# Optimization experiments

Hardware: AMD Instinct MI355X
Metric: run time of the kernel (lower is better)

The kernel has to match this reference:

```python
import jax, jax.numpy as jnp
import numpy as np

N_TAU = 100  # steps per delay: dt = tau / N_TAU (backward code uses dt = 0.01*tau)


def F_model(x, y, t, W1, W2, b):
    # F(x(t), x(t - tau), t); t enters the signature but this Model is autonomous,
    # matching the repo's example models.
    return jnp.tanh(W1 @ x + W2 @ y + b)


def setup_inputs() -> dict:
    key = jax.random.key(0)
    d = 512
    k1, k2, k3, k4 = jax.random.split(key, 4)
    scale = 1.0 / np.sqrt(d).astype(np.float32)
    x_0 = jax.random.normal(k1, (d,), dtype=jnp.float32)
    W1 = jax.random.normal(k2, (d, d), dtype=jnp.float32) * scale
    W2 = jax.random.normal(k3, (d, d), dtype=jnp.float32) * scale
    b = jax.random.normal(k4, (d,), dtype=jnp.float32)
    tau = jnp.ones((), dtype=jnp.float32)  # time delay; dt = 0.01 * tau
    N = 2000  # = floor(T / dt) with T = 20, tau = 1
    return {"x_0": x_0, "tau": tau, "W1": W1, "W2": W2, "b": b, "N": N}


def reference(x_0, tau, W1, W2, b, N):
    """Forward-Euler DDE solve of x'(t) = F(x(t), x(t - tau), t), x(t) = x_0 for t <= 0.
    Returns the trajectory as a [d, N+1] array (kth column = state at step k),
    matching DDE_Solver's x_Trajectory layout."""
    d = x_0.shape[0]
    M = N_TAU + 1  # ring buffer holds the last N_tau+1 states
    dt = 0.01 * tau

    buf0 = jnp.zeros((d, M), dtype=x_0.dtype).at[:, 0].set(x_0)

    def step(buf, j):
        x_j = buf[:, j % M]
        # delayed state x(t_j - tau) = x_{j - N_tau}; (j - N_tau) % M == (j + 1) % M
        y_hist = buf[:, (j + 1) % M]
        y_j = jnp.where(j >= N_TAU, y_hist, x_0)  # pre-history: x(t) = x_0
        t_j = j * dt
        x_jp1 = x_j + dt * F_model(x_j, y_j, t_j, W1, W2, b)
        buf = buf.at[:, (j + 1) % M].set(x_jp1)
        return buf, x_jp1

    _, ys = jax.lax.scan(step, buf0, jnp.arange(N))  # ys: [N, d]
    return jnp.concatenate([x_0[:, None], ys.T], axis=1)  # [d, N+1]
```

## Files before the change

kernel.cpp:

```cpp
#include <hip/hip_runtime.h>


#define D    512
#define NTAU 100
#define M    112
#define NWGS 128

typedef unsigned long long u64;

__device__ __forceinline__ float lo_f(u64 v){ union{unsigned u; float f;} c; c.u=(unsigned)v; return c.f; }
__device__ __forceinline__ u64 pack_rec(unsigned tag, float x){ union{unsigned u; float f;} c; c.f=x; return ((u64)tag<<32)|(u64)c.u; }
__device__ __forceinline__ u64 ag_ld(const u64* p){
    return __hip_atomic_load(p, __ATOMIC_RELAXED, __HIP_MEMORY_SCOPE_AGENT);
}
__device__ __forceinline__ void ag_st(u64* p, u64 v){
    __hip_atomic_store(p, v, __ATOMIC_RELAXED, __HIP_MEMORY_SCOPE_AGENT);
}

__global__ __launch_bounds__(64, 1) void ndde_r4(
    const float* __restrict__ x0p, const float* __restrict__ taup,
    const float* __restrict__ W1,  const float* __restrict__ W2,
    const float* __restrict__ bb,  const int* __restrict__ Np,
    float* __restrict__ out, u64* __restrict__ ring)
{
    const int lane    = threadIdx.x & 63;
    const int rowbase = blockIdx.x * 4;
    const int N       = Np[0];
    const float dt    = 0.01f * taup[0];

    float w1v[4][8], w2v[4][8];
    #pragma unroll
    for (int r = 0; r < 4; ++r){
        const float* p1 = W1 + (size_t)(rowbase + r) * D + lane;
        const float* p2 = W2 + (size_t)(rowbase + r) * D + lane;
        #pragma unroll
        for (int i = 0; i < 8; ++i){
            w1v[r][i] = p1[64 * i];
            w2v[r][i] = p2[64 * i];
        }
    }
    #pragma unroll
    for (int r = 0; r < 4; ++r){
        #pragma unroll
        for (int i = 0; i < 8; ++i)
            asm volatile("" : "+v"(w1v[r][i]), "+v"(w2v[r][i]));
    }

    float xv0[8];
    #pragma unroll
    for (int i = 0; i < 8; ++i) xv0[i] = x0p[64 * i + lane];
    float yp[4], a0, a1, a2, a3;
    {
        float t[4];
        #pragma unroll
        for (int r = 0; r < 4; ++r){
            float sy = 0.f, st = 0.f;
            #pragma unroll
            for (int i = 0; i < 8; ++i){
                sy = fmaf(w2v[r][i], xv0[i], sy);
                st = fmaf(w1v[r][i], xv0[i], st);
            }
            yp[r] = sy; t[r] = st;
        }
        a0 = t[0] + yp[0]; a1 = t[1] + yp[1];
        a2 = t[2] + yp[2]; a3 = t[3] + yp[3];
    }
    #pragma unroll
    for (int off = 32; off >= 1; off >>= 1){
        a0 += __shfl_xor(a0, off, 64);
        a1 += __shfl_xor(a1, off, 64);
        a2 += __shfl_xor(a2, off, 64);
        a3 += __shfl_xor(a3, off, 64);
    }

    float xloc = 0.f, bval = 0.f;
    if (lane < 4){
        const int row = rowbase + lane;
        xloc = x0p[row];
        bval = bb[row];
        out[(size_t)row * (N + 1)] = xloc;
        if (N >= 1){
            const float acc = (lane == 0) ? a0 : (lane == 1) ? a1
                            : (lane == 2) ? a2 : a3;
            const float x1 = xloc + dt * tanhf(acc + bval);
            xloc = x1;
            ag_st(ring + D + row, pack_rec(2u, x1));
            out[(size_t)row * (N + 1) + 1] = x1;
        }
    }

    u64 xr[8], yr[8];
    int sx = 1, sp = 2, sy = 1;
    bool dead = false;

    for (int j = 1; j < N && !dead; ++j){
        const bool needy  = (j > NTAU);
        const unsigned tx = (unsigned)(j + 1);
        const u64* px = ring + (size_t)sx * D + lane;

        if (needy){
            const u64* py = ring + (size_t)sy * D + lane;
            #pragma unroll
            for (int i = 0; i < 8; ++i) yr[i] = ag_ld(py + 64 * i);
        }

        int it = 0;
        for (;;){
            #pragma unroll
            for (int i = 0; i < 8; ++i) xr[i] = ag_ld(px + 64 * i);
            bool ok = true;
            #pragma unroll
            for (int i = 0; i < 8; ++i) ok &= ((unsigned)(xr[i] >> 32) == tx);
            if (__all(ok)) break;
            if (++it > (1 << 22)){ dead = true; break; }
        }

        if (needy){
            const unsigned ty = (unsigned)(j - NTAU + 1);
            bool ok = true;
            #pragma unroll
            for (int i = 0; i < 8; ++i) ok &= ((unsigned)(yr[i] >> 32) == ty);
            if (!__all(ok)){
                const u64* py = ring + (size_t)sy * D + lane;
                int it2 = 0;
                for (;;){
                    #pragma unroll
                    for (int i = 0; i < 8; ++i) yr[i] = ag_ld(py + 64 * i);
                    bool ok2 = true;
                    #pragma unroll
                    for (int i = 0; i < 8; ++i) ok2 &= ((unsigned)(yr[i] >> 32) == ty);
                    if (__all(ok2)) break;
                    if (++it2 > (1 << 22)){ dead = true; break; }
                }
            }
        }

        if (needy){
            a0 = a1 = a2 = a3 = 0.f;
            #pragma unroll
            for (int i = 0; i < 8; ++i){
                const float xf = lo_f(xr[i]), yf = lo_f(yr[i]);
                a0 = fmaf(w1v[0][i], xf, a0); a0 = fmaf(w2v[0][i], yf, a0);
                a1 = fmaf(w1v[1][i], xf, a1); a1 = fmaf(w2v[1][i], yf, a1);
                a2 = fmaf(w1v[2][i], xf, a2); a2 = fmaf(w2v[2][i], yf, a2);
                a3 = fmaf(w1v[3][i], xf, a3); a3 = fmaf(w2v[3][i], yf, a3);
            }
        } else {
            a0 = yp[0]; a1 = yp[1]; a2 = yp[2]; a3 = yp[3];
            #pragma unroll
            for (int i = 0; i < 8; ++i){
                const float xf = lo_f(xr[i]);
                a0 = fmaf(w1v[0][i], xf, a0);
                a1 = fmaf(w1v[1][i], xf, a1);
                a2 = fmaf(w1v[2][i], xf, a2);
                a3 = fmaf(w1v[3][i], xf, a3);
            }
        }

        #pragma unroll
        for (int off = 32; off >= 1; off >>= 1){
            a0 += __shfl_xor(a0, off, 64);
            a1 += __shfl_xor(a1, off, 64);
            a2 += __shfl_xor(a2, off, 64);
            a3 += __shfl_xor(a3, off, 64);
        }

        if (lane < 4){
            const float acc = (lane == 0) ? a0 : (lane == 1) ? a1
                            : (lane == 2) ? a2 : a3;
            const float xn = xloc + dt * tanhf(acc + bval);
            xloc = xn;
            const int row = rowbase + lane;
            ag_st(ring + (size_t)sp * D + row, pack_rec(tx + 1, xn));
            out[(size_t)row * (N + 1) + (j + 1)] = xn;
        }

        sx = (sx == M - 1) ? 0 : sx + 1;
        sp = (sp == M - 1) ? 0 : sp + 1;
        if (j >= NTAU + 1) sy = (sy == M - 1) ? 0 : sy + 1;
    }
}

extern "C" void kernel_launch(void* const* d_in, const int* in_sizes, int n_in,
                              void* d_out, int out_size, void* d_ws, size_t ws_size,
                              hipStream_t stream)
{
    const float* x0  = (const float*)d_in[0];
    const float* tau = (const float*)d_in[1];
    const float* W1  = (const float*)d_in[2];
    const float* W2  = (const float*)d_in[3];
    const float* b   = (const float*)d_in[4];
    const int*   Np  = (const int*)  d_in[5];

    u64* ring = (u64*)d_ws;

    hipLaunchKernelGGL(ndde_r4, dim3(NWGS), dim3(64), 0, stream,
                       x0, tau, W1, W2, b, Np, (float*)d_out, ring);
}
```

Before: 3.627 ms.

## Halve workgroups to 64 with 8 rows each and precompute delayed term locally

Each workgroup now owns 8 rows instead of 4, so 64 workgroups take part in the per-step spin-wait synchronization instead of 128. Each workgroup also keeps a private copy of recent states in workspace and computes the W2·y delayed contribution off the critical path after publishing its new state. This removes the second polled ring read from the step's critical path. The cost is twice the register footprint for the weights and twice the per-lane dot-product work per step, plus extra global writes and reads for the private history. The spin-timeout limits are also lowered.

```diff
diff --git a/kernel.cpp b/kernel.cpp
--- a/kernel.cpp
+++ b/kernel.cpp
@@ -1,10 +1,11 @@
 #include <hip/hip_runtime.h>
 
 
-#define D    512
-#define NTAU 100
-#define M    112
-#define NWGS 128
+#define D     512
+#define NTAU  100
+#define M     112
+#define HSLOT 101
+#define NW    64
 
 typedef unsigned long long u64;
 
@@ -16,21 +17,31 @@
 __device__ __forceinline__ void ag_st(u64* p, u64 v){
     __hip_atomic_store(p, v, __ATOMIC_RELAXED, __HIP_MEMORY_SCOPE_AGENT);
 }
-
-__global__ __launch_bounds__(64, 1) void ndde_r4(
+__device__ __forceinline__ float sel8(const float* a, int k){
+    float s = a[0];
+    s = (k == 1) ? a[1] : s;  s = (k == 2) ? a[2] : s;
+    s = (k == 3) ? a[3] : s;  s = (k == 4) ? a[4] : s;
+    s = (k == 5) ? a[5] : s;  s = (k == 6) ? a[6] : s;
+    s = (k == 7) ? a[7] : s;
+    return s;
+}
+
+__global__ __launch_bounds__(64, 1) void ndde_r5(
     const float* __restrict__ x0p, const float* __restrict__ taup,
     const float* __restrict__ W1,  const float* __restrict__ W2,
     const float* __restrict__ bb,  const int* __restrict__ Np,
-    float* __restrict__ out, u64* __restrict__ ring)
+    float* __restrict__ out, u64* __restrict__ ring,
+    float* __restrict__ hist, int use_hist)
 {
     const int lane    = threadIdx.x & 63;
-    const int rowbase = blockIdx.x * 4;
+    const int wb      = blockIdx.x;
+    const int rowbase = wb * 8;
     const int N       = Np[0];
     const float dt    = 0.01f * taup[0];
 
-    float w1v[4][8], w2v[4][8];
-    #pragma unroll
-    for (int r = 0; r < 4; ++r){
+    float w1v[8][8], w2v[8][8];
+    #pragma unroll
+    for (int r = 0; r < 8; ++r){
         const float* p1 = W1 + (size_t)(rowbase + r) * D + lane;
         const float* p2 = W2 + (size_t)(rowbase + r) * D + lane;
         #pragma unroll
@@ -40,7 +51,7 @@
         }
     }
     #pragma unroll
-    for (int r = 0; r < 4; ++r){
+    for (int r = 0; r < 8; ++r){
         #pragma unroll
         for (int i = 0; i < 8; ++i)
             asm volatile("" : "+v"(w1v[r][i]), "+v"(w2v[r][i]));
@@ -49,48 +60,43 @@
     float xv0[8];
     #pragma unroll
     for (int i = 0; i < 8; ++i) xv0[i] = x0p[64 * i + lane];
-    float yp[4], a0, a1, a2, a3;
-    {
-        float t[4];
-        #pragma unroll
-        for (int r = 0; r < 4; ++r){
-            float sy = 0.f, st = 0.f;
-            #pragma unroll
-            for (int i = 0; i < 8; ++i){
-                sy = fmaf(w2v[r][i], xv0[i], sy);
-                st = fmaf(w1v[r][i], xv0[i], st);
-            }
-            yp[r] = sy; t[r] = st;
-        }
-        a0 = t[0] + yp[0]; a1 = t[1] + yp[1];
-        a2 = t[2] + yp[2]; a3 = t[3] + yp[3];
+    float yp[8], a[8];
+    #pragma unroll
+    for (int r = 0; r < 8; ++r){
+        float sy = 0.f, st = 0.f;
+        #pragma unroll
+        for (int i = 0; i < 8; ++i){
+            sy = fmaf(w2v[r][i], xv0[i], sy);
+            st = fmaf(w1v[r][i], xv0[i], st);
+        }
+        yp[r] = sy; a[r] = st + sy;
     }
     #pragma unroll
     for (int off = 32; off >= 1; off >>= 1){
-        a0 += __shfl_xor(a0, off, 64);
-        a1 += __shfl_xor(a1, off, 64);
-        a2 += __shfl_xor(a2, off, 64);
-        a3 += __shfl_xor(a3, off, 64);
+        #pragma unroll
+        for (int r = 0; r < 8; ++r) a[r] += __shfl_xor(a[r], off, 64);
     }
 
     float xloc = 0.f, bval = 0.f;
-    if (lane < 4){
+    if (lane < 8){
         const int row = rowbase + lane;
         xloc = x0p[row];
         bval = bb[row];
         out[(size_t)row * (N + 1)] = xloc;
         if (N >= 1){
-            const float acc = (lane == 0) ? a0 : (lane == 1) ? a1
-                            : (lane == 2) ? a2 : a3;
-            const float x1 = xloc + dt * tanhf(acc + bval);
+            const float x1 = xloc + dt * tanhf(sel8(a, lane) + bval);
             xloc = x1;
             ag_st(ring + D + row, pack_rec(2u, x1));
             out[(size_t)row * (N + 1) + 1] = x1;
         }
     }
 
-    u64 xr[8], yr[8];
-    int sx = 1, sp = 2, sy = 1;
+    float* myh = hist + (size_t)wb * HSLOT * D;
+
+    u64 xr[8];
+    float xf[8];
+    int sx = 1, sp = 2, syr = 1;
+    int hw = 0, hr = 0;
     bool dead = false;
 
     for (int j = 1; j < N && !dead; ++j){
@@ -98,8 +104,9 @@
         const unsigned tx = (unsigned)(j + 1);
         const u64* px = ring + (size_t)sx * D + lane;
 
-        if (needy){
-            const u64* py = ring + (size_t)sy * D + lane;
+        u64 yr[8];
+        if (!use_hist && needy){
+            const u64* py = ring + (size_t)syr * D + lane;
             #pragma unroll
             for (int i = 0; i < 8; ++i) yr[i] = ag_ld(py + 64 * i);
         }
@@ -112,16 +119,18 @@
             #pragma unroll
             for (int i = 0; i < 8; ++i) ok &= ((unsigned)(xr[i] >> 32) == tx);
             if (__all(ok)) break;
-            if (++it > (1 << 22)){ dead = true; break; }
-        }
-
-        if (needy){
+            if (++it > (1 << 20)){ dead = true; break; }
+        }
+        #pragma unroll
+        for (int i = 0; i < 8; ++i) xf[i] = lo_f(xr[i]);
+
+        if (!use_hist && needy){
             const unsigned ty = (unsigned)(j - NTAU + 1);
             bool ok = true;
             #pragma unroll
             for (int i = 0; i < 8; ++i) ok &= ((unsigned)(yr[i] >> 32) == ty);
             if (!__all(ok)){
-                const u64* py = ring + (size_t)sy * D + lane;
+                const u64* py = ring + (size_t)syr * D + lane;
                 int it2 = 0;
                 for (;;){
                     #pragma unroll
@@ -130,54 +139,62 @@
                     #pragma unroll
                     for (int i = 0; i < 8; ++i) ok2 &= ((unsigned)(yr[i] >> 32) == ty);
                     if (__all(ok2)) break;
-                    if (++it2 > (1 << 22)){ dead = true; break; }
+                    if (++it2 > (1 << 20)){ dead = true; break; }
                 }
             }
-        }
-
-        if (needy){
-            a0 = a1 = a2 = a3 = 0.f;
-            #pragma unroll
-            for (int i = 0; i < 8; ++i){
-                const float xf = lo_f(xr[i]), yf = lo_f(yr[i]);
-                a0 = fmaf(w1v[0][i], xf, a0); a0 = fmaf(w2v[0][i], yf, a0);
-                a1 = fmaf(w1v[1][i], xf, a1); a1 = fmaf(w2v[1][i], yf, a1);
-                a2 = fmaf(w1v[2][i], xf, a2); a2 = fmaf(w2v[2][i], yf, a2);
-                a3 = fmaf(w1v[3][i], xf, a3); a3 = fmaf(w2v[3][i], yf, a3);
+            #pragma unroll
+            for (int r = 0; r < 8; ++r){
+                float sy = 0.f;
+                #pragma unroll
+                for (int i = 0; i < 8; ++i) sy = fmaf(w2v[r][i], lo_f(yr[i]), sy);
+                yp[r] = sy;
             }
-        } else {
-            a0 = yp[0]; a1 = yp[1]; a2 = yp[2]; a3 = yp[3];
-            #pragma unroll
-            for (int i = 0; i < 8; ++i){
-                const float xf = lo_f(xr[i]);
-                a0 = fmaf(w1v[0][i], xf, a0);
-                a1 = fmaf(w1v[1][i], xf, a1);
-                a2 = fmaf(w1v[2][i], xf, a2);
-                a3 = fmaf(w1v[3][i], xf, a3);
-            }
-        }
-
+        }
+
+        #pragma unroll
+        for (int r = 0; r < 8; ++r){
+            float s = yp[r];
+            #pragma unroll
+            for (int i = 0; i < 8; ++i) s = fmaf(w1v[r][i], xf[i], s);
+            a[r] = s;
+        }
         #pragma unroll
         for (int off = 32; off >= 1; off >>= 1){
-            a0 += __shfl_xor(a0, off, 64);
-            a1 += __shfl_xor(a1, off, 64);
-            a2 += __shfl_xor(a2, off, 64);
-            a3 += __shfl_xor(a3, off, 64);
-        }
-
-        if (lane < 4){
-            const float acc = (lane == 0) ? a0 : (lane == 1) ? a1
-                            : (lane == 2) ? a2 : a3;
-            const float xn = xloc + dt * tanhf(acc + bval);
+            #pragma unroll
+            for (int r = 0; r < 8; ++r) a[r] += __shfl_xor(a[r], off, 64);
+        }
+        if (lane < 8){
+            const float xn = xloc + dt * tanhf(sel8(a, lane) + bval);
             xloc = xn;
             const int row = rowbase + lane;
             ag_st(ring + (size_t)sp * D + row, pack_rec(tx + 1, xn));
             out[(size_t)row * (N + 1) + (j + 1)] = xn;
         }
 
+        if (use_hist){
+            float* hwp = myh + (size_t)hw * D + lane;
+            #pragma unroll
+            for (int i = 0; i < 8; ++i) hwp[64 * i] = xf[i];
+            if (j >= NTAU){
+                const float* hrp = myh + (size_t)hr * D + lane;
+                float yv[8];
+                #pragma unroll
+                for (int i = 0; i < 8; ++i) yv[i] = hrp[64 * i];
+                #pragma unroll
+                for (int r = 0; r < 8; ++r){
+                    float sy = 0.f;
+                    #pragma unroll
+                    for (int i = 0; i < 8; ++i) sy = fmaf(w2v[r][i], yv[i], sy);
+                    yp[r] = sy;
+                }
+                hr = (hr == HSLOT - 1) ? 0 : hr + 1;
+            }
+            hw = (hw == HSLOT - 1) ? 0 : hw + 1;
+        }
+
         sx = (sx == M - 1) ? 0 : sx + 1;
         sp = (sp == M - 1) ? 0 : sp + 1;
-        if (j >= NTAU + 1) sy = (sy == M - 1) ? 0 : sy + 1;
+        if (j >= NTAU + 1) syr = (syr == M - 1) ? 0 : syr + 1;
     }
 }
 
@@ -192,8 +209,13 @@
     const float* b   = (const float*)d_in[4];
     const int*   Np  = (const int*)  d_in[5];
 
-    u64* ring = (u64*)d_ws;
-
-    hipLaunchKernelGGL(ndde_r4, dim3(NWGS), dim3(64), 0, stream,
-                       x0, tau, W1, W2, b, Np, (float*)d_out, ring);
-}
+    const size_t ring_bytes = (size_t)M * D * 8;
+    const size_t hist_bytes = (size_t)NW * HSLOT * D * 4;
+    const int use_hist = (ws_size >= ring_bytes + hist_bytes) ? 1 : 0;
+
+    u64*   ring = (u64*)d_ws;
+    float* hist = (float*)((char*)d_ws + ring_bytes);
+
+    hipLaunchKernelGGL(ndde_r5, dim3(NW), dim3(64), 0, stream,
+                       x0, tau, W1, W2, b, Np, (float*)d_out, ring, hist, use_hist);
+}
```

New measurement: 2.961 ms. 18.4% less time.
